# Kernel optimization log

Measured on AMD Instinct MI355X. Metric: run time of the kernel, lower is better.

Reference implementation:

```python
import jax, jax.numpy as jnp
import numpy as np

D_MODEL = 1024
D_STATE = 16
D_CONV = 4
EXPAND = 2
D_INNER = EXPAND * D_MODEL        # 2048
DT_RANK = D_MODEL // 16           # ceil(1024/16) = 64
B, L = 2, 2048


def setup_inputs() -> dict:
    key = jax.random.key(0)
    ks = jax.random.split(key, 8)
    def init(k, shape, fan_in):
        return jax.random.normal(k, shape, jnp.float32) / np.sqrt(fan_in).astype(np.float32)
    x = jax.random.normal(ks[0], (B, L, D_MODEL), jnp.float32)
    W_in = init(ks[1], (2 * D_INNER, D_MODEL), D_MODEL)
    conv_w = init(ks[2], (D_INNER, 1, D_CONV), D_CONV)      # depthwise kernel (O, I/groups, K)
    conv_b = jnp.zeros((D_INNER,), jnp.float32)
    W_x = init(ks[3], (DT_RANK + 2 * D_STATE, D_INNER), D_INNER)
    W_dt = init(ks[4], (D_INNER, DT_RANK), DT_RANK)
    b_dt = jnp.zeros((D_INNER,), jnp.float32)
    A_log = jnp.log(jnp.tile(jnp.arange(1, D_STATE + 1, dtype=jnp.float32), (D_INNER, 1)))
    D_param = jnp.ones((D_INNER,), jnp.float32)
    W_out = init(ks[5], (D_MODEL, D_INNER), D_INNER)
    return {"x": x, "W_in": W_in, "conv_w": conv_w, "conv_b": conv_b,
            "W_x": W_x, "W_dt": W_dt, "b_dt": b_dt, "A_log": A_log,
            "D_param": D_param, "W_out": W_out}


def _mamba_forward(x, W_in, conv_w, conv_b, W_x, W_dt, b_dt, A_log, D_param, W_out):
    b, l, d = x.shape
    # in_proj -> split into ssm path and gate residual
    x_and_res = x @ W_in.T                               # [b, l, 2*d_inner]
    x_m, res = jnp.split(x_and_res, 2, axis=-1)
    # causal depthwise conv1d (torch pads both sides d_conv-1 then slices [:l] == left-pad causal conv)
    xc = jnp.transpose(x_m, (0, 2, 1))                   # [b, d_inner, l]
    xc = jax.lax.conv_general_dilated(
        xc, conv_w, window_strides=(1,), padding=[(D_CONV - 1, 0)],
        dimension_numbers=('NCH', 'OIH', 'NCH'), feature_group_count=D_INNER)
    xc = xc + conv_b[None, :, None]
    x_m = jax.nn.silu(jnp.transpose(xc, (0, 2, 1)))      # [b, l, d_inner]
    # ssm parameterization
    A = -jnp.exp(A_log)                                  # [d_inner, n]
    x_dbl = x_m @ W_x.T                                  # [b, l, dt_rank + 2n]
    dlt, Bm, Cm = jnp.split(x_dbl, [DT_RANK, DT_RANK + D_STATE], axis=-1)
    delta = jax.nn.softplus(dlt @ W_dt.T + b_dt)         # [b, l, d_inner]
    # selective scan over time
    def step(h, inp):
        d_i, B_i, C_i, x_i = inp                         # [b,d_in], [b,n], [b,n], [b,d_in]
        dA = jnp.exp(d_i[..., None] * A)                 # [b, d_in, n]
        h = dA * h + (d_i * x_i)[..., None] * B_i[:, None, :]
        y = jnp.einsum('bdn,bn->bd', h, C_i)
        return h, y
    h0 = jnp.zeros((b, D_INNER, D_STATE), x.dtype)
    seq = (jnp.transpose(delta, (1, 0, 2)), jnp.transpose(Bm, (1, 0, 2)),
           jnp.transpose(Cm, (1, 0, 2)), jnp.transpose(x_m, (1, 0, 2)))
    _, ys = jax.lax.scan(step, h0, seq)                  # [l, b, d_inner]
    y = jnp.transpose(ys, (1, 0, 2)) + D_param * x_m     # [b, l, d_inner]
    y = y * jax.nn.silu(res)
    return y @ W_out.T                                   # [b, l, d_model]


def reference(x, W_in, conv_w, conv_b, W_x, W_dt, b_dt, A_log, D_param, W_out):
    return _mamba_forward(x, W_in, conv_w, conv_b, W_x, W_dt, b_dt, A_log, D_param, W_out)
```

## Files before the change

kernel.cpp:

```cpp
#include <hip/hip_runtime.h>

typedef unsigned short u16;
typedef __attribute__((ext_vector_type(8))) short bf16x8;
typedef __attribute__((ext_vector_type(4))) float f32x4;

#define B_SZ   2
#define L_SZ   2048
#define DM     1024
#define DI     2048
#define NST    16
#define RNK    64
#define TOK    (B_SZ * L_SZ)
#define NC     128
#define CLEN   (L_SZ / NC)
#define XDS    128
#define KSPL   8

__device__ __forceinline__ float bf2f(u16 u) {
    return __uint_as_float(((unsigned int)u) << 16);
}
__device__ __forceinline__ u16 f2bf(float f) {
    unsigned int x = __float_as_uint(f);
    x += 0x7fffu + ((x >> 16) & 1u);
    return (u16)(x >> 16);
}
__device__ __forceinline__ float silu(float v) {
    return v / (1.f + __expf(-v));
}
__device__ __forceinline__ float softplus_f(float v) {
    const float r = __logf(1.f + __expf(v));
    return (v > 20.f) ? v : r;
}
__device__ __forceinline__ void gload16(const u16* g, u16* l) {
    __builtin_amdgcn_global_load_lds(
        (const __attribute__((address_space(1))) void*)g,
        (__attribute__((address_space(3))) void*)l, 16, 0, 0);
}
__device__ __forceinline__ ushort4 cvt4(const float4 v) {
    ushort4 o;
    o.x = f2bf(v.x); o.y = f2bf(v.y); o.z = f2bf(v.z); o.w = f2bf(v.w);
    return o;
}

#define Q_XB   1048576
#define Q_WIN  (Q_XB + 1048576)
#define Q_WOUT (Q_WIN + 524288)
#define Q_WX   (Q_WOUT + 65536)
#define Q_WDT  (Q_WX + 32768)
__global__ __launch_bounds__(256)
void cvt_all(const float4* __restrict__ x,  const float4* __restrict__ Wi,
             const float4* __restrict__ Wo, const float4* __restrict__ Wx,
             const float4* __restrict__ Wd,
             ushort4* __restrict__ xb,  ushort4* __restrict__ Wib,
             ushort4* __restrict__ Wob, ushort4* __restrict__ Wxb,
             ushort4* __restrict__ Wdb)
{
    const int i = blockIdx.x * 256 + threadIdx.x;
    if (i < Q_XB) {
        xb[i] = cvt4(x[i]);
    } else if (i < Q_WIN) {
        const int j = i - Q_XB;  Wib[j] = cvt4(Wi[j]);
    } else if (i < Q_WOUT) {
        const int j = i - Q_WIN; Wob[j] = cvt4(Wo[j]);
    } else if (i < Q_WX) {
        const int j = i - Q_WOUT;
        const int row = (j * 4) >> 11;
        if (row < 96) Wxb[j] = cvt4(Wx[j]);
        else          Wxb[j] = (ushort4){0, 0, 0, 0};
    } else if (i < Q_WDT) {
        const int j = i - Q_WX;  Wdb[j] = cvt4(Wd[j]);
    }
}

__global__ __launch_bounds__(256, 2)
void gemm_in(const u16* __restrict__ A, const u16* __restrict__ B,
             u16* __restrict__ out0, u16* __restrict__ out1)
{
    const int K = DM, N = 2 * DI;
    __shared__ u16 sA[128 * 32];
    __shared__ u16 sB[128 * 32];

    const int tid  = threadIdx.x;
    const int rowBase = blockIdx.x << 7;
    const int colBase = blockIdx.y << 7;
    const int wave = tid >> 6, lane = tid & 63;
    const int wm = (wave >> 1) << 6;
    const int wn = (wave & 1) << 6;
    const int lrow = lane & 15, quad = lane >> 4;

    const int sr  = tid >> 2;
    const int skc = tid & 3;
    const u16* Ap = A + (size_t)(rowBase + sr) * K + skc * 8;
    const u16* Bp = B + (size_t)(colBase + sr) * K + skc * 8;
    const size_t rowJump = (size_t)64 * K;
    u16* lA0 = &sA[tid * 8];
    u16* lA1 = &sA[64 * 32 + tid * 8];
    u16* lB0 = &sB[tid * 8];
    u16* lB1 = &sB[64 * 32 + tid * 8];

    f32x4 acc[4][4];
#pragma unroll
    for (int i = 0; i < 4; ++i)
#pragma unroll
        for (int j = 0; j < 4; ++j) acc[i][j] = (f32x4){0.f, 0.f, 0.f, 0.f};

    const int KT = K >> 5;
    for (int kt = 0; kt < KT; ++kt) {
        const int ko = kt * 32;
        gload16(Ap + ko, lA0);
        gload16(Ap + ko + rowJump, lA1);
        gload16(Bp + ko, lB0);
        gload16(Bp + ko + rowJump, lB1);
        __syncthreads();

        bf16x8 af[4], bfr[4];
#pragma unroll
        for (int i = 0; i < 4; ++i)
            af[i] = *(const bf16x8*)&sA[(wm + i * 16 + lrow) * 32 + quad * 8];
#pragma unroll
        for (int j = 0; j < 4; ++j)
            bfr[j] = *(const bf16x8*)&sB[(wn + j * 16 + lrow) * 32 + quad * 8];

#pragma unroll
        for (int i = 0; i < 4; ++i)
#pragma unroll
            for (int j = 0; j < 4; ++j)
                acc[i][j] = __builtin_amdgcn_mfma_f32_16x16x32_bf16(
                    bfr[j], af[i], acc[i][j], 0, 0, 0);
        __syncthreads();
    }

#pragma unroll
    for (int i = 0; i < 4; ++i) {
        const int token = rowBase + wm + i * 16 + lrow;
#pragma unroll
        for (int j = 0; j < 4; ++j) {
            const int ch = colBase + wn + j * 16 + quad * 4;
            const f32x4 v = acc[i][j];
            if (ch < DI) {
                ushort4 o;
                o.x = f2bf(v[0]); o.y = f2bf(v[1]);
                o.z = f2bf(v[2]); o.w = f2bf(v[3]);
                *(ushort4*)&out0[(size_t)token * DI + ch] = o;
            } else {
                ushort4 o;
                o.x = f2bf(silu(v[0])); o.y = f2bf(silu(v[1]));
                o.z = f2bf(silu(v[2])); o.w = f2bf(silu(v[3]));
                *(ushort4*)&out1[(size_t)token * DI + (ch - DI)] = o;
            }
        }
    }
}

template<int EPI>
__global__ __launch_bounds__(256, 2)
void gemm_mt64(const u16* __restrict__ A, const u16* __restrict__ B,
               const int K, const int N,
               u16* __restrict__ out0, float* __restrict__ outF,
               const float* __restrict__ bias)
{
    __shared__ u16 sA[64 * 32];
    __shared__ u16 sB[128 * 32];

    const int tid  = threadIdx.x;
    const int rowBase = blockIdx.x << 6;
    const int colBase = blockIdx.y << 7;
    const int wave = tid >> 6, lane = tid & 63;
    const int wm = (wave >> 1) << 5;
    const int wn = (wave & 1) << 6;
    const int lrow = lane & 15, quad = lane >> 4;

    const int sr  = tid >> 2;
    const int skc = tid & 3;
    const u16* Ap = A + (size_t)(rowBase + sr) * K + skc * 8;
    const u16* Bp = B + (size_t)(colBase + sr) * K + skc * 8;
    const size_t rowJump = (size_t)64 * K;
    u16* lA0 = &sA[tid * 8];
    u16* lB0 = &sB[tid * 8];
    u16* lB1 = &sB[64 * 32 + tid * 8];

    f32x4 acc[2][4];
#pragma unroll
    for (int i = 0; i < 2; ++i)
#pragma unroll
        for (int j = 0; j < 4; ++j) acc[i][j] = (f32x4){0.f, 0.f, 0.f, 0.f};

    const int KT = K >> 5;
    for (int kt = 0; kt < KT; ++kt) {
        const int ko = kt * 32;
        gload16(Ap + ko, lA0);
        gload16(Bp + ko, lB0);
        gload16(Bp + ko + rowJump, lB1);
        __syncthreads();

        bf16x8 af[2], bfr[4];
#pragma unroll
        for (int i = 0; i < 2; ++i)
            af[i] = *(const bf16x8*)&sA[(wm + i * 16 + lrow) * 32 + quad * 8];
#pragma unroll
        for (int j = 0; j < 4; ++j)
            bfr[j] = *(const bf16x8*)&sB[(wn + j * 16 + lrow) * 32 + quad * 8];

#pragma unroll
        for (int i = 0; i < 2; ++i)
#pragma unroll
            for (int j = 0; j < 4; ++j)
                acc[i][j] = __builtin_amdgcn_mfma_f32_16x16x32_bf16(
                    bfr[j], af[i], acc[i][j], 0, 0, 0);
        __syncthreads();
    }

#pragma unroll
    for (int i = 0; i < 2; ++i) {
        const int token = rowBase + wm + i * 16 + lrow;
#pragma unroll
        for (int j = 0; j < 4; ++j) {
            const int ch = colBase + wn + j * 16 + quad * 4;
            const f32x4 v = acc[i][j];
            if (EPI == 0) {
                *(float4*)&outF[(size_t)token * N + ch] =
                    (float4){v[0], v[1], v[2], v[3]};
            } else {
                const float4 bb = *(const float4*)&bias[ch];
                ushort4 o;
                o.x = f2bf(softplus_f(v[0] + bb.x));
                o.y = f2bf(softplus_f(v[1] + bb.y));
                o.z = f2bf(softplus_f(v[2] + bb.z));
                o.w = f2bf(softplus_f(v[3] + bb.w));
                *(ushort4*)&out0[(size_t)token * N + ch] = o;
            }
        }
    }
}

__global__ __launch_bounds__(256, 4)
void gemm_delta(const u16* __restrict__ A, const u16* __restrict__ B,
                u16* __restrict__ out0, const float* __restrict__ bias)
{
    const int K = RNK;
    __shared__ u16 sA[2][64 * 32];
    __shared__ u16 sB[2][128 * 32];

    const int tid  = threadIdx.x;
    const int rowBase = blockIdx.x << 6;
    const int colBase = blockIdx.y << 7;
    const int wave = tid >> 6, lane = tid & 63;
    const int wm = (wave >> 1) << 5;
    const int wn = (wave & 1) << 6;
    const int lrow = lane & 15, quad = lane >> 4;

    const int sr  = tid >> 2;
    const int skc = tid & 3;
    const u16* Ap = A + (size_t)(rowBase + sr) * K + skc * 8;
    const u16* Bp = B + (size_t)(colBase + sr) * K + skc * 8;
    const size_t rowJump = (size_t)64 * K;

    gload16(Ap,                &sA[0][tid * 8]);
    gload16(Ap + 32,           &sA[1][tid * 8]);
    gload16(Bp,                &sB[0][tid * 8]);
    gload16(Bp + 32,           &sB[1][tid * 8]);
    gload16(Bp + rowJump,      &sB[0][64 * 32 + tid * 8]);
    gload16(Bp + rowJump + 32, &sB[1][64 * 32 + tid * 8]);

    f32x4 acc[2][4];
#pragma unroll
    for (int i = 0; i < 2; ++i)
#pragma unroll
        for (int j = 0; j < 4; ++j) acc[i][j] = (f32x4){0.f, 0.f, 0.f, 0.f};

    __syncthreads();

#pragma unroll
    for (int kc = 0; kc < 2; ++kc) {
        bf16x8 af[2], bfr[4];
#pragma unroll
        for (int i = 0; i < 2; ++i)
            af[i] = *(const bf16x8*)&sA[kc][(wm + i * 16 + lrow) * 32 + quad * 8];
#pragma unroll
        for (int j = 0; j < 4; ++j)
            bfr[j] = *(const bf16x8*)&sB[kc][(wn + j * 16 + lrow) * 32 + quad * 8];

#pragma unroll
        for (int i = 0; i < 2; ++i)
#pragma unroll
            for (int j = 0; j < 4; ++j)
                acc[i][j] = __builtin_amdgcn_mfma_f32_16x16x32_bf16(
                    bfr[j], af[i], acc[i][j], 0, 0, 0);
    }

#pragma unroll
    for (int i = 0; i < 2; ++i) {
        const int token = rowBase + wm + i * 16 + lrow;
#pragma unroll
        for (int j = 0; j < 4; ++j) {
            const int ch = colBase + wn + j * 16 + quad * 4;
            const f32x4 v = acc[i][j];
            const float4 bb = *(const float4*)&bias[ch];
            ushort4 o;
            o.x = f2bf(softplus_f(v[0] + bb.x));
            o.y = f2bf(softplus_f(v[1] + bb.y));
            o.z = f2bf(softplus_f(v[2] + bb.z));
            o.w = f2bf(softplus_f(v[3] + bb.w));
            *(ushort4*)&out0[(size_t)token * DI + ch] = o;
        }
    }
}

__global__ __launch_bounds__(256, 2)
void gemm_xdbl(const u16* __restrict__ A, const u16* __restrict__ B,
               float* __restrict__ part)
{
    __shared__ u16 sA[128 * 32];
    __shared__ u16 sB[128 * 32];

    const int tid  = threadIdx.x;
    const int rowBase = blockIdx.x << 7;
    const int ks   = blockIdx.y;
    const int k0   = ks * (DI / KSPL);
    const int wave = tid >> 6, lane = tid & 63;
    const int wm = (wave >> 1) << 6;
    const int wn = (wave & 1) << 6;
    const int lrow = lane & 15, quad = lane >> 4;

    const int sr  = tid >> 2;
    const int skc = tid & 3;
    const u16* Ap = A + (size_t)(rowBase + sr) * DI + k0 + skc * 8;
    const u16* Bp = B + (size_t)sr * DI + k0 + skc * 8;
    const size_t rowJump = (size_t)64 * DI;
    u16* lA0 = &sA[tid * 8];
    u16* lA1 = &sA[64 * 32 + tid * 8];
    u16* lB0 = &sB[tid * 8];
    u16* lB1 = &sB[64 * 32 + tid * 8];

    f32x4 acc[4][4];
#pragma unroll
    for (int i = 0; i < 4; ++i)
#pragma unroll
        for (int j = 0; j < 4; ++j) acc[i][j] = (f32x4){0.f, 0.f, 0.f, 0.f};

    const int KT = (DI / KSPL) >> 5;
    for (int kt = 0; kt < KT; ++kt) {
        const int ko = kt * 32;
        gload16(Ap + ko, lA0);
        gload16(Ap + ko + rowJump, lA1);
        gload16(Bp + ko, lB0);
        gload16(Bp + ko + rowJump, lB1);
        __syncthreads();

        bf16x8 af[4], bfr[4];
#pragma unroll
        for (int i = 0; i < 4; ++i)
            af[i] = *(const bf16x8*)&sA[(wm + i * 16 + lrow) * 32 + quad * 8];
#pragma unroll
        for (int j = 0; j < 4; ++j)
            bfr[j] = *(const bf16x8*)&sB[(wn + j * 16 + lrow) * 32 + quad * 8];

#pragma unroll
        for (int i = 0; i < 4; ++i)
#pragma unroll
            for (int j = 0; j < 4; ++j)
                acc[i][j] = __builtin_amdgcn_mfma_f32_16x16x32_bf16(
                    bfr[j], af[i], acc[i][j], 0, 0, 0);
        __syncthreads();
    }

    float* base = part + (size_t)ks * TOK * XDS;
#pragma unroll
    for (int i = 0; i < 4; ++i) {
        const int token = rowBase + wm + i * 16 + lrow;
#pragma unroll
        for (int j = 0; j < 4; ++j) {
            const int ch = wn + j * 16 + quad * 4;
            const f32x4 v = acc[i][j];
            *(float4*)&base[(size_t)token * XDS + ch] =
                (float4){v[0], v[1], v[2], v[3]};
        }
    }
}

__global__ __launch_bounds__(256)
void reduce_part(const float4* __restrict__ part, float4* __restrict__ xdbl,
                 u16* __restrict__ dltB)
{
    const int i = blockIdx.x * 256 + threadIdx.x;
    const int n4 = TOK * XDS / 4;
    float4 s = part[i];
#pragma unroll
    for (int ks = 1; ks < KSPL; ++ks) {
        const float4 v = part[(size_t)ks * n4 + i];
        s.x += v.x; s.y += v.y; s.z += v.z; s.w += v.w;
    }
    xdbl[i] = s;
    const int col4 = (i & (XDS / 4 - 1)) * 4;
    if (col4 < RNK) {
        const int row = i >> 5;
        *(ushort4*)(dltB + (size_t)row * RNK + col4) = cvt4(s);
    }
}

__global__ __launch_bounds__(256)
void conv_silu_kernel(const u16* __restrict__ xm, const float* __restrict__ cw,
                      const float* __restrict__ cb, u16* __restrict__ xc)
{
    const int idx = blockIdx.x * 256 + threadIdx.x;
    const int ch  = (idx & (DI / 4 - 1)) * 4;
    const int t   = idx >> 9;
    const int l   = t & (L_SZ - 1);

    const float4 w0 = ((const float4*)cw)[ch];
    const float4 w1 = ((const float4*)cw)[ch + 1];
    const float4 w2 = ((const float4*)cw)[ch + 2];
    const float4 w3 = ((const float4*)cw)[ch + 3];
    const float4 bb = *(const float4*)(cb + ch);
    float a0 = bb.x, a1 = bb.y, a2 = bb.z, a3 = bb.w;

    const u16* base = xm + (size_t)t * DI + ch;
    if (l >= 3) {
        const ushort4 v = *(const ushort4*)(base - 3 * DI);
        a0 += w0.x * bf2f(v.x); a1 += w1.x * bf2f(v.y);
        a2 += w2.x * bf2f(v.z); a3 += w3.x * bf2f(v.w);
    }
    if (l >= 2) {
        const ushort4 v = *(const ushort4*)(base - 2 * DI);
        a0 += w0.y * bf2f(v.x); a1 += w1.y * bf2f(v.y);
        a2 += w2.y * bf2f(v.z); a3 += w3.y * bf2f(v.w);
    }
    if (l >= 1) {
        const ushort4 v = *(const ushort4*)(base - DI);
        a0 += w0.z * bf2f(v.x); a1 += w1.z * bf2f(v.y);
        a2 += w2.z * bf2f(v.z); a3 += w3.z * bf2f(v.w);
    }
    {
        const ushort4 v = *(const ushort4*)(base);
        a0 += w0.w * bf2f(v.x); a1 += w1.w * bf2f(v.y);
        a2 += w2.w * bf2f(v.z); a3 += w3.w * bf2f(v.w);
    }
    ushort4 o;
    o.x = f2bf(silu(a0)); o.y = f2bf(silu(a1));
    o.z = f2bf(silu(a2)); o.w = f2bf(silu(a3));
    *(ushort4*)(xc + (size_t)t * DI + ch) = o;
}

__global__ __launch_bounds__(256)
void scan_pass1(const u16* __restrict__ dlt16, const float* __restrict__ xdbl,
                const u16* __restrict__ xc, const float* __restrict__ A_log,
                u16* __restrict__ hfin, float* __restrict__ Ssum)
{
    const int tid = threadIdx.x;
    const int ch  = blockIdx.x * 256 + tid;
    const int b   = blockIdx.y / NC;
    const int c   = blockIdx.y % NC;
    const int t0  = b * L_SZ + c * CLEN;

    __shared__ float sB[CLEN][16];
    {
        const int i = tid >> 4, nn = tid & 15;
        sB[i][nn] = xdbl[(size_t)(t0 + i) * XDS + 64 + nn];
    }

    float A[16];
    {
        const float4* Ar = (const float4*)(A_log + (size_t)ch * 16);
#pragma unroll
        for (int k = 0; k < 4; ++k) {
            const float4 v = Ar[k];
            A[4*k+0] = -__expf(v.x); A[4*k+1] = -__expf(v.y);
            A[4*k+2] = -__expf(v.z); A[4*k+3] = -__expf(v.w);
        }
    }
    __syncthreads();

    float h[16];
#pragma unroll
    for (int n = 0; n < 16; ++n) h[n] = 0.f;
    float S = 0.f;

    const u16* dp  = dlt16 + (size_t)t0 * DI + ch;
    const u16* xcp = xc    + (size_t)t0 * DI + ch;
    float d  = bf2f(*dp);
    float xv = bf2f(*xcp);

    for (int i = 0; i < CLEN; ++i) {
        const float dn = bf2f(dp[DI]);
        const float xn = bf2f(xcp[DI]);
        const float dx = d * xv;
        S += d;
#pragma unroll
        for (int k = 0; k < 4; ++k) {
            const float4 Bv = *(const float4*)&sB[i][k * 4];
#pragma unroll
            for (int j = 0; j < 4; ++j) {
                const int n = k * 4 + j;
                const float e = __expf(d * A[n]);
                h[n] = e * h[n] + dx * (&Bv.x)[j];
            }
        }
        dp += DI; xcp += DI;
        d = dn; xv = xn;
    }

    u16* hp = hfin + ((size_t)(b * NC + c) * DI + ch) * 16;
#pragma unroll
    for (int k = 0; k < 4; ++k) {
        ushort4 o;
        o.x = f2bf(h[4*k]); o.y = f2bf(h[4*k+1]);
        o.z = f2bf(h[4*k+2]); o.w = f2bf(h[4*k+3]);
        *(ushort4*)(hp + 4 * k) = o;
    }
    Ssum[(size_t)(b * NC + c) * DI + ch] = S;
}

__global__ __launch_bounds__(256)
void scan_combine(const u16* __restrict__ hfin, const float* __restrict__ Ssum,
                  const float* __restrict__ A_log, u16* __restrict__ h0buf)
{
    const int idx  = blockIdx.x * 256 + threadIdx.x;
    const int b    = idx >> 15;
    const int base = idx & 32767;
    const int ch   = base >> 4;
    const float A  = -__expf(A_log[base]);

    const u16* hp  = hfin  + (size_t)b * NC * 32768 + base;
    const float* Sp = Ssum + (size_t)b * NC * DI + ch;
    u16* op        = h0buf + (size_t)b * NC * 32768 + base;

    float h0 = 0.f;
#pragma unroll 4
    for (int c = 0; c < NC; ++c) {
        *op = f2bf(h0);
        h0 = bf2f(*hp) + __expf(A * (*Sp)) * h0;
        hp += 32768; Sp += DI; op += 32768;
    }
}

__global__ __launch_bounds__(256)
void scan_pass2(const u16* __restrict__ dlt16, const float* __restrict__ xdbl,
                const u16* __restrict__ xc, const u16* __restrict__ sres,
                const float* __restrict__ A_log, const float* __restrict__ Dp,
                const u16* __restrict__ h0buf, u16* __restrict__ yfin)
{
    const int tid = threadIdx.x;
    const int ch  = blockIdx.x * 256 + tid;
    const int b   = blockIdx.y / NC;
    const int c   = blockIdx.y % NC;
    const int t0  = b * L_SZ + c * CLEN;

    __shared__ float sB[CLEN][16], sC[CLEN][16];
    {
        const int i = tid >> 4, nn = tid & 15;
        sB[i][nn] = xdbl[(size_t)(t0 + i) * XDS + 64 + nn];
        sC[i][nn] = xdbl[(size_t)(t0 + i) * XDS + 80 + nn];
    }

    float A[16];
    {
        const float4* Ar = (const float4*)(A_log + (size_t)ch * 16);
#pragma unroll
        for (int k = 0; k < 4; ++k) {
            const float4 v = Ar[k];
            A[4*k+0] = -__expf(v.x); A[4*k+1] = -__expf(v.y);
            A[4*k+2] = -__expf(v.z); A[4*k+3] = -__expf(v.w);
        }
    }
    const float Dval = Dp[ch];

    float h[16];
    {
        const u16* hp = h0buf + (size_t)(b * NC + c) * 32768 + (size_t)ch * 16;
#pragma unroll
        for (int k = 0; k < 4; ++k) {
            const ushort4 q = *(const ushort4*)(hp + 4 * k);
            h[4*k+0] = bf2f(q.x); h[4*k+1] = bf2f(q.y);
            h[4*k+2] = bf2f(q.z); h[4*k+3] = bf2f(q.w);
        }
    }
    __syncthreads();

    const u16* dp  = dlt16 + (size_t)t0 * DI + ch;
    const u16* xcp = xc    + (size_t)t0 * DI + ch;
    const u16* srp = sres  + (size_t)t0 * DI + ch;
    u16* yp        = yfin  + (size_t)t0 * DI + ch;
    float d  = bf2f(*dp);
    float xv = bf2f(*xcp);
    float rv = bf2f(*srp);

    for (int i = 0; i < CLEN; ++i) {
        const float dn = bf2f(dp[DI]);
        const float xn = bf2f(xcp[DI]);
        const float rn = bf2f(srp[DI]);
        const float dx = d * xv;
        float acc0 = 0.f, acc1 = 0.f, acc2 = 0.f, acc3 = 0.f;
#pragma unroll
        for (int k = 0; k < 4; ++k) {
            const float4 Bv = *(const float4*)&sB[i][k * 4];
            const float4 Cv = *(const float4*)&sC[i][k * 4];
#pragma unroll
            for (int j = 0; j < 4; ++j) {
                const int n = k * 4 + j;
                const float e = __expf(d * A[n]);
                h[n] = e * h[n] + dx * (&Bv.x)[j];
                const float t = h[n] * (&Cv.x)[j];
                if (j == 0) acc0 += t; else if (j == 1) acc1 += t;
                else if (j == 2) acc2 += t; else acc3 += t;
            }
        }
        const float p = (acc0 + acc1) + (acc2 + acc3);
        const float y = (p + Dval * xv) * rv;
        *yp = f2bf(y);
        dp += DI; xcp += DI; srp += DI; yp += DI;
        d = dn; xv = xn; rv = rn;
    }
}

extern "C" void kernel_launch(void* const* d_in, const int* in_sizes, int n_in,
                              void* d_out, int out_size, void* d_ws, size_t ws_size,
                              hipStream_t stream)
{
    const float* x      = (const float*)d_in[0];
    const float* W_in   = (const float*)d_in[1];
    const float* conv_w = (const float*)d_in[2];
    const float* conv_b = (const float*)d_in[3];
    const float* W_x    = (const float*)d_in[4];
    const float* W_dt   = (const float*)d_in[5];
    const float* b_dt   = (const float*)d_in[6];
    const float* A_log  = (const float*)d_in[7];
    const float* D_par  = (const float*)d_in[8];
    const float* W_out  = (const float*)d_in[9];
    float* out = (float*)d_out;

    char* ws = (char*)d_ws;
    size_t off = 0;
    u16* xb    = (u16*)(ws + off); off += (size_t)TOK * DM * 2;
    u16* Winb  = (u16*)(ws + off); off += (size_t)(2 * DI) * DM * 2;
    u16* Woutb = (u16*)(ws + off); off += (size_t)DM * DI * 2;
    u16* Wxb   = (u16*)(ws + off); off += (size_t)XDS * DI * 2;
    u16* Wdtb  = (u16*)(ws + off); off += (size_t)DI * RNK * 2;
    u16* dltB  = (u16*)(ws + off); off += (size_t)TOK * RNK * 2;
    u16* xm    = (u16*)(ws + off); off += (size_t)TOK * DI * 2;
    u16* xc    = (u16*)(ws + off); off += (size_t)TOK * DI * 2;
    u16* sres  = (u16*)(ws + off); off += (size_t)TOK * DI * 2;
    float* xdblP = (float*)(ws + off); off += (size_t)TOK * XDS * 4;
    u16* dlt16   = (u16*)(ws + off);   off += (size_t)TOK * DI * 2;
    u16* hfin    = (u16*)(ws + off);   off += (size_t)NC * B_SZ * DI * NST * 2;
    u16* h0buf   = (u16*)(ws + off);   off += (size_t)NC * B_SZ * DI * NST * 2;
    float* Ssum  = (float*)(ws + off); off += (size_t)NC * B_SZ * DI * 4;
    u16* yfin = xm;
    float* part = (float*)hfin;

    cvt_all<<<(Q_WDT + 255) / 256, 256, 0, stream>>>(
        (const float4*)x, (const float4*)W_in, (const float4*)W_out,
        (const float4*)W_x, (const float4*)W_dt,
        (ushort4*)xb, (ushort4*)Winb, (ushort4*)Woutb,
        (ushort4*)Wxb, (ushort4*)Wdtb);

    gemm_in<<<dim3(TOK / 128, (2 * DI) / 128), 256, 0, stream>>>(
        xb, Winb, xm, sres);

    conv_silu_kernel<<<(TOK * DI / 4) / 256, 256, 0, stream>>>(xm, conv_w, conv_b, xc);

    gemm_xdbl<<<dim3(TOK / 128, KSPL), 256, 0, stream>>>(xc, Wxb, part);
    reduce_part<<<(TOK * XDS / 4) / 256, 256, 0, stream>>>(
        (const float4*)part, (float4*)xdblP, dltB);

    gemm_delta<<<dim3(TOK / 64, DI / 128), 256, 0, stream>>>(
        dltB, Wdtb, dlt16, b_dt);

    scan_pass1<<<dim3(DI / 256, B_SZ * NC), 256, 0, stream>>>(
        dlt16, xdblP, xc, A_log, hfin, Ssum);
    scan_combine<<<(B_SZ * DI * NST) / 256, 256, 0, stream>>>(
        hfin, Ssum, A_log, h0buf);
    scan_pass2<<<dim3(DI / 256, B_SZ * NC), 256, 0, stream>>>(
        dlt16, xdblP, xc, sres, A_log, D_par, h0buf, yfin);

    gemm_mt64<0><<<dim3(TOK / 64, DM / 128), 256, 0, stream>>>(
        yfin, Woutb, DI, DM, nullptr, out, nullptr);
}
```

Before: 306.3 us.

## Double-buffer LDS staging in GEMMs and halve scan chunk count

Adds two-stage LDS double buffering to the in-proj, mt64 and xdbl GEMMs, so the global-to-LDS load of the next K tile overlaps MFMA work on the current tile. It also halves the number of scan chunks from 128 to 64, which doubles the chunk length, and makes the shared-memory loads of B and C loop to cover longer chunks. Fewer chunks means less carry-state traffic between scan passes but less parallelism per pass. Double buffering doubles LDS use per block, which may lower occupancy.

```diff
diff --git a/kernel.cpp b/kernel.cpp
--- a/kernel.cpp
+++ b/kernel.cpp
@@ -11,7 +11,8 @@
 #define NST    16
 #define RNK    64
 #define TOK    (B_SZ * L_SZ)
-#define NC     128
+#define NC     64
+#define NCMAX  128
 #define CLEN   (L_SZ / NC)
 #define XDS    128
 #define KSPL   8
@@ -40,6 +41,44 @@
     ushort4 o;
     o.x = f2bf(v.x); o.y = f2bf(v.y); o.z = f2bf(v.z); o.w = f2bf(v.w);
     return o;
+}
+
+__device__ __forceinline__ void mfma_4x4(const u16* sAb, const u16* sBb,
+                                         int wm, int wn, int lrow, int quad,
+                                         f32x4 (&acc)[4][4])
+{
+    bf16x8 af[4], bfr[4];
+#pragma unroll
+    for (int i = 0; i < 4; ++i)
+        af[i] = *(const bf16x8*)&sAb[(wm + i * 16 + lrow) * 32 + quad * 8];
+#pragma unroll
+    for (int j = 0; j < 4; ++j)
+        bfr[j] = *(const bf16x8*)&sBb[(wn + j * 16 + lrow) * 32 + quad * 8];
+#pragma unroll
+    for (int i = 0; i < 4; ++i)
+#pragma unroll
+        for (int j = 0; j < 4; ++j)
+            acc[i][j] = __builtin_amdgcn_mfma_f32_16x16x32_bf16(
+                bfr[j], af[i], acc[i][j], 0, 0, 0);
+}
+
+__device__ __forceinline__ void mfma_2x4(const u16* sAb, const u16* sBb,
+                                         int wm, int wn, int lrow, int quad,
+                                         f32x4 (&acc)[2][4])
+{
+    bf16x8 af[2], bfr[4];
+#pragma unroll
+    for (int i = 0; i < 2; ++i)
+        af[i] = *(const bf16x8*)&sAb[(wm + i * 16 + lrow) * 32 + quad * 8];
+#pragma unroll
+    for (int j = 0; j < 4; ++j)
+        bfr[j] = *(const bf16x8*)&sBb[(wn + j * 16 + lrow) * 32 + quad * 8];
+#pragma unroll
+    for (int i = 0; i < 2; ++i)
+#pragma unroll
+        for (int j = 0; j < 4; ++j)
+            acc[i][j] = __builtin_amdgcn_mfma_f32_16x16x32_bf16(
+                bfr[j], af[i], acc[i][j], 0, 0, 0);
 }
 
 #define Q_XB   1048576
@@ -76,9 +115,9 @@
 void gemm_in(const u16* __restrict__ A, const u16* __restrict__ B,
              u16* __restrict__ out0, u16* __restrict__ out1)
 {
-    const int K = DM, N = 2 * DI;
-    __shared__ u16 sA[128 * 32];
-    __shared__ u16 sB[128 * 32];
+    const int K = DM;
+    __shared__ u16 sA[2][128 * 32];
+    __shared__ u16 sB[2][128 * 32];
 
     const int tid  = threadIdx.x;
     const int rowBase = blockIdx.x << 7;
@@ -93,10 +132,14 @@
     const u16* Ap = A + (size_t)(rowBase + sr) * K + skc * 8;
     const u16* Bp = B + (size_t)(colBase + sr) * K + skc * 8;
     const size_t rowJump = (size_t)64 * K;
-    u16* lA0 = &sA[tid * 8];
-    u16* lA1 = &sA[64 * 32 + tid * 8];
-    u16* lB0 = &sB[tid * 8];
-    u16* lB1 = &sB[64 * 32 + tid * 8];
+
+#define STAGE_IN(bf, kt) do {                                   \
+        const int _ko = (kt) * 32;                              \
+        gload16(Ap + _ko,           &sA[bf][tid * 8]);          \
+        gload16(Ap + _ko + rowJump, &sA[bf][64*32 + tid * 8]);  \
+        gload16(Bp + _ko,           &sB[bf][tid * 8]);          \
+        gload16(Bp + _ko + rowJump, &sB[bf][64*32 + tid * 8]);  \
+    } while (0)
 
     f32x4 acc[4][4];
 #pragma unroll
@@ -105,30 +148,17 @@
         for (int j = 0; j < 4; ++j) acc[i][j] = (f32x4){0.f, 0.f, 0.f, 0.f};
 
     const int KT = K >> 5;
-    for (int kt = 0; kt < KT; ++kt) {
-        const int ko = kt * 32;
-        gload16(Ap + ko, lA0);
-        gload16(Ap + ko + rowJump, lA1);
-        gload16(Bp + ko, lB0);
-        gload16(Bp + ko + rowJump, lB1);
+    STAGE_IN(0, 0);
+    __syncthreads();
+    for (int kt = 0; kt < KT; kt += 2) {
+        if (kt + 1 < KT) STAGE_IN(1, kt + 1);
+        mfma_4x4(&sA[0][0], &sB[0][0], wm, wn, lrow, quad, acc);
         __syncthreads();
-
-        bf16x8 af[4], bfr[4];
-#pragma unroll
-        for (int i = 0; i < 4; ++i)
-            af[i] = *(const bf16x8*)&sA[(wm + i * 16 + lrow) * 32 + quad * 8];
-#pragma unroll
-        for (int j = 0; j < 4; ++j)
-            bfr[j] = *(const bf16x8*)&sB[(wn + j * 16 + lrow) * 32 + quad * 8];
-
-#pragma unroll
-        for (int i = 0; i < 4; ++i)
-#pragma unroll
-            for (int j = 0; j < 4; ++j)
-                acc[i][j] = __builtin_amdgcn_mfma_f32_16x16x32_bf16(
-                    bfr[j], af[i], acc[i][j], 0, 0, 0);
+        if (kt + 2 < KT) STAGE_IN(0, kt + 2);
+        mfma_4x4(&sA[1][0], &sB[1][0], wm, wn, lrow, quad, acc);
         __syncthreads();
     }
+#undef STAGE_IN
 
 #pragma unroll
     for (int i = 0; i < 4; ++i) {
@@ -159,8 +189,8 @@
                u16* __restrict__ out0, float* __restrict__ outF,
                const float* __restrict__ bias)
 {
-    __shared__ u16 sA[64 * 32];
-    __shared__ u16 sB[128 * 32];
+    __shared__ u16 sA[2][64 * 32];
+    __shared__ u16 sB[2][128 * 32];
 
     const int tid  = threadIdx.x;
     const int rowBase = blockIdx.x << 6;
@@ -175,9 +205,13 @@
     const u16* Ap = A + (size_t)(rowBase + sr) * K + skc * 8;
     const u16* Bp = B + (size_t)(colBase + sr) * K + skc * 8;
     const size_t rowJump = (size_t)64 * K;
-    u16* lA0 = &sA[tid * 8];
-    u16* lB0 = &sB[tid * 8];
-    u16* lB1 = &sB[64 * 32 + tid * 8];
+
+#define STAGE_MT(bf, kt) do {                                   \
+        const int _ko = (kt) * 32;                              \
+        gload16(Ap + _ko,           &sA[bf][tid * 8]);          \
+        gload16(Bp + _ko,           &sB[bf][tid * 8]);          \
+        gload16(Bp + _ko + rowJump, &sB[bf][64*32 + tid * 8]);  \
+    } while (0)
 
     f32x4 acc[2][4];
 #pragma unroll
@@ -186,29 +220,17 @@
         for (int j = 0; j < 4; ++j) acc[i][j] = (f32x4){0.f, 0.f, 0.f, 0.f};
 
     const int KT = K >> 5;
-    for (int kt = 0; kt < KT; ++kt) {
-        const int ko = kt * 32;
-        gload16(Ap + ko, lA0);
-        gload16(Bp + ko, lB0);
-        gload16(Bp + ko + rowJump, lB1);
+    STAGE_MT(0, 0);
+    __syncthreads();
+    for (int kt = 0; kt < KT; kt += 2) {
+        if (kt + 1 < KT) STAGE_MT(1, kt + 1);
+        mfma_2x4(&sA[0][0], &sB[0][0], wm, wn, lrow, quad, acc);
         __syncthreads();
-
-        bf16x8 af[2], bfr[4];
-#pragma unroll
-        for (int i = 0; i < 2; ++i)
-            af[i] = *(const bf16x8*)&sA[(wm + i * 16 + lrow) * 32 + quad * 8];
-#pragma unroll
-        for (int j = 0; j < 4; ++j)
-            bfr[j] = *(const bf16x8*)&sB[(wn + j * 16 + lrow) * 32 + quad * 8];
-
-#pragma unroll
-        for (int i = 0; i < 2; ++i)
-#pragma unroll
-            for (int j = 0; j < 4; ++j)
-                acc[i][j] = __builtin_amdgcn_mfma_f32_16x16x32_bf16(
-                    bfr[j], af[i], acc[i][j], 0, 0, 0);
+        if (kt + 2 < KT) STAGE_MT(0, kt + 2);
+        mfma_2x4(&sA[1][0], &sB[1][0], wm, wn, lrow, quad, acc);
         __syncthreads();
     }
+#undef STAGE_MT
 
 #pragma unroll
     for (int i = 0; i < 2; ++i) {
@@ -271,22 +293,8 @@
     __syncthreads();
 
 #pragma unroll
-    for (int kc = 0; kc < 2; ++kc) {
-        bf16x8 af[2], bfr[4];
-#pragma unroll
-        for (int i = 0; i < 2; ++i)
-            af[i] = *(const bf16x8*)&sA[kc][(wm + i * 16 + lrow) * 32 + quad * 8];
-#pragma unroll
-        for (int j = 0; j < 4; ++j)
-            bfr[j] = *(const bf16x8*)&sB[kc][(wn + j * 16 + lrow) * 32 + quad * 8];
-
-#pragma unroll
-        for (int i = 0; i < 2; ++i)
-#pragma unroll
-            for (int j = 0; j < 4; ++j)
-                acc[i][j] = __builtin_amdgcn_mfma_f32_16x16x32_bf16(
-                    bfr[j], af[i], acc[i][j], 0, 0, 0);
-    }
+    for (int kc = 0; kc < 2; ++kc)
+        mfma_2x4(&sA[kc][0], &sB[kc][0], wm, wn, lrow, quad, acc);
 
 #pragma unroll
     for (int i = 0; i < 2; ++i) {
@@ -310,8 +318,8 @@
 void gemm_xdbl(const u16* __restrict__ A, const u16* __restrict__ B,
                float* __restrict__ part)
 {
-    __shared__ u16 sA[128 * 32];
-    __shared__ u16 sB[128 * 32];
+    __shared__ u16 sA[2][128 * 32];
+    __shared__ u16 sB[2][128 * 32];
 
     const int tid  = threadIdx.x;
     const int rowBase = blockIdx.x << 7;
@@ -327,10 +335,14 @@
     const u16* Ap = A + (size_t)(rowBase + sr) * DI + k0 + skc * 8;
     const u16* Bp = B + (size_t)sr * DI + k0 + skc * 8;
     const size_t rowJump = (size_t)64 * DI;
-    u16* lA0 = &sA[tid * 8];
-    u16* lA1 = &sA[64 * 32 + tid * 8];
-    u16* lB0 = &sB[tid * 8];
-    u16* lB1 = &sB[64 * 32 + tid * 8];
+
+#define STAGE_XD(bf, kt) do {                                   \
+        const int _ko = (kt) * 32;                              \
+        gload16(Ap + _ko,           &sA[bf][tid * 8]);          \
+        gload16(Ap + _ko + rowJump, &sA[bf][64*32 + tid * 8]);  \
+        gload16(Bp + _ko,           &sB[bf][tid * 8]);          \
+        gload16(Bp + _ko + rowJump, &sB[bf][64*32 + tid * 8]);  \
+    } while (0)
 
     f32x4 acc[4][4];
 #pragma unroll
@@ -339,30 +351,17 @@
         for (int j = 0; j < 4; ++j) acc[i][j] = (f32x4){0.f, 0.f, 0.f, 0.f};
 
     const int KT = (DI / KSPL) >> 5;
-    for (int kt = 0; kt < KT; ++kt) {
-        const int ko = kt * 32;
-        gload16(Ap + ko, lA0);
-        gload16(Ap + ko + rowJump, lA1);
-        gload16(Bp + ko, lB0);
-        gload16(Bp + ko + rowJump, lB1);
+    STAGE_XD(0, 0);
+    __syncthreads();
+    for (int kt = 0; kt < KT; kt += 2) {
+        if (kt + 1 < KT) STAGE_XD(1, kt + 1);
+        mfma_4x4(&sA[0][0], &sB[0][0], wm, wn, lrow, quad, acc);
         __syncthreads();
-
-        bf16x8 af[4], bfr[4];
-#pragma unroll
-        for (int i = 0; i < 4; ++i)
-            af[i] = *(const bf16x8*)&sA[(wm + i * 16 + lrow) * 32 + quad * 8];
-#pragma unroll
-        for (int j = 0; j < 4; ++j)
-            bfr[j] = *(const bf16x8*)&sB[(wn + j * 16 + lrow) * 32 + quad * 8];
-
-#pragma unroll
-        for (int i = 0; i < 4; ++i)
-#pragma unroll
-            for (int j = 0; j < 4; ++j)
-                acc[i][j] = __builtin_amdgcn_mfma_f32_16x16x32_bf16(
-                    bfr[j], af[i], acc[i][j], 0, 0, 0);
+        if (kt + 2 < KT) STAGE_XD(0, kt + 2);
+        mfma_4x4(&sA[1][0], &sB[1][0], wm, wn, lrow, quad, acc);
         __syncthreads();
     }
+#undef STAGE_XD
 
     float* base = part + (size_t)ks * TOK * XDS;
 #pragma unroll
@@ -453,10 +452,9 @@
     const int t0  = b * L_SZ + c * CLEN;
 
     __shared__ float sB[CLEN][16];
-    {
-        const int i = tid >> 4, nn = tid & 15;
-        sB[i][nn] = xdbl[(size_t)(t0 + i) * XDS + 64 + nn];
-    }
+#pragma unroll
+    for (int r = tid; r < CLEN * 16; r += 256)
+        sB[r >> 4][r & 15] = xdbl[(size_t)(t0 + (r >> 4)) * XDS + 64 + (r & 15)];
 
     float A[16];
     {
@@ -546,10 +544,10 @@
     const int t0  = b * L_SZ + c * CLEN;
 
     __shared__ float sB[CLEN][16], sC[CLEN][16];
-    {
-        const int i = tid >> 4, nn = tid & 15;
-        sB[i][nn] = xdbl[(size_t)(t0 + i) * XDS + 64 + nn];
-        sC[i][nn] = xdbl[(size_t)(t0 + i) * XDS + 80 + nn];
+#pragma unroll
+    for (int r = tid; r < CLEN * 16; r += 256) {
+        sB[r >> 4][r & 15] = xdbl[(size_t)(t0 + (r >> 4)) * XDS + 64 + (r & 15)];
+        sC[r >> 4][r & 15] = xdbl[(size_t)(t0 + (r >> 4)) * XDS + 80 + (r & 15)];
     }
 
     float A[16];
@@ -641,9 +639,9 @@
     u16* sres  = (u16*)(ws + off); off += (size_t)TOK * DI * 2;
     float* xdblP = (float*)(ws + off); off += (size_t)TOK * XDS * 4;
     u16* dlt16   = (u16*)(ws + off);   off += (size_t)TOK * DI * 2;
-    u16* hfin    = (u16*)(ws + off);   off += (size_t)NC * B_SZ * DI * NST * 2;
-    u16* h0buf   = (u16*)(ws + off);   off += (size_t)NC * B_SZ * DI * NST * 2;
-    float* Ssum  = (float*)(ws + off); off += (size_t)NC * B_SZ * DI * 4;
+    u16* hfin    = (u16*)(ws + off);   off += (size_t)NCMAX * B_SZ * DI * NST * 2;
+    u16* h0buf   = (u16*)(ws + off);   off += (size_t)NCMAX * B_SZ * DI * NST * 2;
+    float* Ssum  = (float*)(ws + off); off += (size_t)NCMAX * B_SZ * DI * 4;
     u16* yfin = xm;
     float* part = (float*)hfin;
 
```

Result: no change. 307.2 us (+0.3%).
